# Kernel optimization log

Measured on AMD Instinct MI355X. Metric: run time of the kernel, lower is better.

Reference implementation:

```python
import jax, jax.numpy as jnp
import numpy as np

HIDDEN_DIM = 512
SCALE = float(np.sqrt(HIDDEN_DIM))  # hidden_dim ** 0.5, matches torch


def setup_inputs() -> dict:
    key = jax.random.key(0)
    ks = jax.random.split(key, 4)
    B, S, D_IN = 8, 4096, 64
    x = jax.random.normal(ks[0], (B, S, D_IN), dtype=jnp.float32)
    # Linear weights stored as [in, out] (transposed vs torch's [out, in])
    Wq = jax.random.normal(ks[1], (D_IN, HIDDEN_DIM), dtype=jnp.float32) * (1.0 / np.sqrt(D_IN))
    Wk = jax.random.normal(ks[2], (D_IN, HIDDEN_DIM), dtype=jnp.float32) * (1.0 / np.sqrt(D_IN))
    Wv = jax.random.normal(ks[3], (D_IN, HIDDEN_DIM), dtype=jnp.float32) * (1.0 / np.sqrt(D_IN))
    bq = jnp.zeros((HIDDEN_DIM,), dtype=jnp.float32)
    bk = jnp.zeros((HIDDEN_DIM,), dtype=jnp.float32)
    bv = jnp.zeros((HIDDEN_DIM,), dtype=jnp.float32)
    return {"x": x, "Wq": Wq, "bq": bq, "Wk": Wk, "bk": bk, "Wv": Wv, "bv": bv}


def reference(x, Wq, bq, Wk, bk, Wv, bv):
    # Q/K/V projections: [B, S, H]
    Q = jnp.einsum('bsd,dh->bsh', x, Wq) + bq
    K = jnp.einsum('bsd,dh->bsh', x, Wk) + bk
    V = jnp.einsum('bsd,dh->bsh', x, Wv) + bv
    # Naive single-head attention with full [B, S, S] score matrix,
    # matching the original torch math exactly.
    scores = jnp.einsum('bqh,bkh->bqk', Q, K) / SCALE
    attn = jax.nn.softmax(scores, axis=-1)
    return jnp.einsum('bqk,bkh->bqh', attn, V)
```

## Files before the change

### kernel.cpp

```cpp
#include <hip/hip_runtime.h>
#include <hip/hip_bf16.h>
#include <math.h>


#define SS 4096
#define DD 64
#define HH 512
#define KSPL 2048

#define CSCALE ((float)(1.4426950408889634 * 0.04419417382415922))

typedef __bf16 bf16x8 __attribute__((ext_vector_type(8)));
typedef float  f32x4  __attribute__((ext_vector_type(4)));
typedef unsigned int u32x4 __attribute__((ext_vector_type(4)));

__device__ __forceinline__ float b2f(__hip_bfloat16 v) { return __bfloat162float(v); }

__device__ __forceinline__ f32x4 mfma16(bf16x8 a, bf16x8 b, f32x4 c) {
  return __builtin_amdgcn_mfma_f32_16x16x32_bf16(a, b, c, 0, 0, 0);
}

__device__ __forceinline__ unsigned pack2(float a, float b) {
  float2 f2; f2.x = a; f2.y = b;
  __hip_bfloat162 h2 = __float22bfloat162_rn(f2);
  unsigned u; __builtin_memcpy(&u, &h2, 4);
  return u;
}

__device__ __forceinline__ float loadf(const void* p, size_t i, int isF32) {
  return isF32 ? ((const float*)p)[i] : b2f(((const __hip_bfloat16*)p)[i]);
}
__device__ __forceinline__ void load8f(const void* p, size_t i, int isF32, float* o) {
  if (isF32) {
    const float4 a = *(const float4*)((const float*)p + i);
    const float4 b = *(const float4*)((const float*)p + i + 4);
    o[0]=a.x; o[1]=a.y; o[2]=a.z; o[3]=a.w; o[4]=b.x; o[5]=b.y; o[6]=b.z; o[7]=b.w;
  } else {
    const bf16x8 v = *(const bf16x8*)((const __hip_bfloat16*)p + i);
#pragma unroll
    for (int k = 0; k < 8; ++k) { __hip_bfloat16 h; __builtin_memcpy(&h, ((const unsigned short*)&v) + k, 2); o[k] = b2f(h); }
  }
}

__global__ void dtype_probe(const void* __restrict__ Wq, int* __restrict__ flag) {
  const unsigned short* h = (const unsigned short*)Wq;
  const int lane = threadIdx.x;
  unsigned int bits = ((unsigned int)h[lane * 2]) << 16;
  float v; __builtin_memcpy(&v, &bits, 4);
  v = fabsf(v);
  if (!isfinite(v) || v > 1e10f) v = 1e10f;
  for (int off = 1; off < 64; off <<= 1) v = fmaxf(v, __shfl_xor(v, off, 64));
  if (lane == 0) *flag = (v > 1e6f) ? 1 : 0;
}

__global__ __launch_bounds__(256) void prep_kernel(
    const void* __restrict__ Wq, const void* __restrict__ Wk,
    const void* __restrict__ Wv, const void* __restrict__ bq,
    const void* __restrict__ bk, __hip_bfloat16* __restrict__ MT,
    float* __restrict__ u, float* __restrict__ w_, float* __restrict__ c_,
    __hip_bfloat16* __restrict__ wvT, const int* __restrict__ flag) {
  const int t = threadIdx.x, blk = blockIdx.x;
  const int isF32 = *flag;
  if (blk < 64) {
    __shared__ float red[256];
    const int i = blk, j = t >> 2, part = t & 3;
    float acc = 0.f, aq[8], ak[8];
    for (int c = 0; c < 16; ++c) {
      load8f(Wq, (size_t)i * HH + part * 128 + c * 8, isF32, aq);
      load8f(Wk, (size_t)j * HH + part * 128 + c * 8, isF32, ak);
#pragma unroll
      for (int k = 0; k < 8; ++k) acc = fmaf(aq[k], ak[k], acc);
    }
    red[t] = acc;
    __syncthreads();
    if (t < 64)
      MT[t * 64 + i] = __float2bfloat16(red[t*4] + red[t*4+1] + red[t*4+2] + red[t*4+3]);
  } else if (blk == 64) {
    __shared__ float pu[256], pw[256], pc[64];
    const int i = t & 63, part = t >> 6;
    float au = 0.f, aw = 0.f, v1[8], v2[8];
    for (int c = 0; c < 16; ++c) {
      load8f(Wq, (size_t)i * HH + part * 128 + c * 8, isF32, v1);
      load8f(bk, part * 128 + c * 8, isF32, v2);
#pragma unroll
      for (int k = 0; k < 8; ++k) au = fmaf(v1[k], v2[k], au);
      load8f(Wk, (size_t)i * HH + part * 128 + c * 8, isF32, v1);
      load8f(bq, part * 128 + c * 8, isF32, v2);
#pragma unroll
      for (int k = 0; k < 8; ++k) aw = fmaf(v1[k], v2[k], aw);
    }
    pu[t] = au; pw[t] = aw;
    if (t < 64) {
      float s = 0.f;
      for (int e = 0; e < 8; ++e)
        s = fmaf(loadf(bq, t * 8 + e, isF32), loadf(bk, t * 8 + e, isF32), s);
      pc[t] = s;
    }
    __syncthreads();
    if (t < 64) {
      u[t]  = pu[t] + pu[t+64] + pu[t+128] + pu[t+192];
      w_[t] = pw[t] + pw[t+64] + pw[t+128] + pw[t+192];
    }
    if (t == 0) {
      float s = 0.f;
      for (int e = 0; e < 64; ++e) s += pc[e];
      *c_ = s;
    }
  } else {
    const int base = (blk - 65) * 2048 + t;
    for (int r = 0; r < 8; ++r) {
      const int e = base + r * 256;
      const int h = e >> 6, d = e & 63;
      wvT[e] = __float2bfloat16(loadf(Wv, (size_t)d * HH + h, isF32));
    }
  }
}

__global__ __launch_bounds__(256) void proj_kernel(
    const void* __restrict__ xraw, const __hip_bfloat16* __restrict__ MT,
    const float* __restrict__ u, const float* __restrict__ w_,
    const float* __restrict__ c_, __hip_bfloat16* __restrict__ xc,
    __hip_bfloat16* __restrict__ y, float* __restrict__ qb,
    float* __restrict__ kb, __hip_bfloat16* __restrict__ xT,
    const int* __restrict__ flag) {
  __shared__ __hip_bfloat16 xs[64 * 72];
  __shared__ __hip_bfloat16 Ms[64 * 72];
  __shared__ float us[64], wl[64];
  __shared__ float cs;

  const int t = threadIdx.x;
  const int isF32 = *flag;
  {
    const int r = t >> 2, cb = (t & 3) * 16;
    *(bf16x8*)(&Ms[r * 72 + cb])     = *(const bf16x8*)(MT + r * 64 + cb);
    *(bf16x8*)(&Ms[r * 72 + cb + 8]) = *(const bf16x8*)(MT + r * 64 + cb + 8);
  }
  if (t < 64) { us[t] = u[t]; wl[t] = w_[t]; }
  if (t == 0) cs = *c_;

  const int b = blockIdx.x & 7;
  const int sbase = (blockIdx.x >> 3) * 64;
  const int rbase = b * SS + sbase;

  for (int i = 0; i < 2; ++i) {
    const int e = i * 256 + t;
    const int row = e >> 3, col = (e & 7) * 8;
    float v[8];
    load8f(xraw, (size_t)(rbase + row) * DD + col, isF32, v);
    __hip_bfloat16* dp = xs + row * 72 + col;
#pragma unroll
    for (int k = 0; k < 8; ++k) dp[k] = __float2bfloat16(v[k]);
  }
  __syncthreads();

  const int wv = t >> 6, lane = t & 63;
  const int l16 = lane & 15, quad = lane >> 4;
  const bf16x8 A0 = *(const bf16x8*)(&xs[(wv * 16 + l16) * 72 + quad * 8]);
  const bf16x8 A1 = *(const bf16x8*)(&xs[(wv * 16 + l16) * 72 + 32 + quad * 8]);
#pragma unroll
  for (int nt = 0; nt < 4; ++nt) {
    const bf16x8 B0 = *(const bf16x8*)(&Ms[(nt * 16 + l16) * 72 + quad * 8]);
    const bf16x8 B1 = *(const bf16x8*)(&Ms[(nt * 16 + l16) * 72 + 32 + quad * 8]);
    f32x4 C = (f32x4){0.f, 0.f, 0.f, 0.f};
    C = mfma16(A0, B0, C);
    C = mfma16(A1, B1, C);
#pragma unroll
    for (int r = 0; r < 4; ++r)
      y[(size_t)(rbase + wv * 16 + quad * 4 + r) * DD + nt * 16 + l16] =
          __float2bfloat16(C[r]);
  }
  if (t < 64) {
    float qa = 0.f, ka = 0.f;
    for (int d = 0; d < 64; ++d) {
      const float xv = b2f(xs[t * 72 + d]);
      qa = fmaf(xv, us[d], qa);
      ka = fmaf(xv, wl[d], ka);
    }
    qb[rbase + t] = (qa + cs) * CSCALE;
    kb[rbase + t] = ka * CSCALE;
  }
  for (int i = 0; i < 2; ++i) {
    const int e = i * 256 + t;
    const int row = e >> 3, col = (e & 7) * 8;
    *(bf16x8*)(xc + (size_t)(rbase + row) * DD + col) = *(const bf16x8*)(xs + row * 72 + col);
  }
  for (int i = 0; i < 16; ++i) {
    const int d = i * 4 + (t >> 6);
    const int sl = t & 63;
    xT[((size_t)b * DD + d) * SS + sbase + sl] = xs[sl * 72 + d];
  }
}

__global__ __launch_bounds__(256) void attn_split(
    const __hip_bfloat16* __restrict__ x,
    const __hip_bfloat16* __restrict__ y,
    const float* __restrict__ qb, const float* __restrict__ kb,
    const __hip_bfloat16* __restrict__ xT,
    float* __restrict__ Opart, float* __restrict__ lpart) {
  __shared__ __hip_bfloat16 xs[2][32 * 72];
  __shared__ __hip_bfloat16 vsm[2][64 * 40];
  const int tid = threadIdx.x;
  const int wv = tid >> 6, lane = tid & 63;
  const int l16 = lane & 15, quad = lane >> 4;
  const int b = blockIdx.x & 7;
  const int ks = (blockIdx.x >> 3) & 1;
  const int qt = (blockIdx.x >> 4) * 4 + wv;
  const int koff = ks * KSPL;
  const size_t rowq = ((size_t)b << 12) + ((size_t)qt << 4);

  const __hip_bfloat16* xb  = x  + ((size_t)b * SS) * DD;
  const __hip_bfloat16* xTb = xT + ((size_t)b * DD) * SS;
  const float* kbb = kb + ((size_t)b * SS);

  const __hip_bfloat16* yp = y + (rowq + l16) * DD + quad * 8;
  const bf16x8 Ylo = *(const bf16x8*)yp;
  const bf16x8 Yhi = *(const bf16x8*)(yp + 32);
  const float qbl = qb[rowq + l16];

  const int sxr = tid >> 3, sxc = (tid & 7) * 8;
  const int taur = (sxr & 3) + ((sxr >> 3) << 2) + (((sxr >> 2) & 1) << 4);
  const int svd = tid >> 2, svc = (tid & 3) * 8;
  const __hip_bfloat16* gx = xb + (size_t)(koff + sxr) * DD + sxc;
  const __hip_bfloat16* gv = xTb + (size_t)svd * SS + koff + svc;
  const float* kbp = kbb + koff + quad * 8;

  bf16x8 nx = *(const bf16x8*)gx;
  bf16x8 nv = *(const bf16x8*)gv;
  *(bf16x8*)(&xs[0][taur * 72 + sxc]) = nx;
  *(bf16x8*)(&vsm[0][svd * 40 + svc]) = nv;
  nx = *(const bf16x8*)(gx + 32 * DD);
  nv = *(const bf16x8*)(gv + 32);
  __syncthreads();

  bf16x8 onesb;
#pragma unroll
  for (int j = 0; j < 8; ++j) onesb[j] = (__bf16)1.0f;

  f32x4 O[4];
#pragma unroll
  for (int n = 0; n < 4; ++n) O[n] = (f32x4){0.f, 0.f, 0.f, 0.f};
  f32x4 Ol = (f32x4){0.f, 0.f, 0.f, 0.f};

  for (int kt = 0; kt < KSPL; kt += 32) {
    const int p = (kt >> 5) & 1, np = p ^ 1;
    if (kt + 32 < KSPL) {
      *(bf16x8*)(&xs[np][taur * 72 + sxc]) = nx;
      *(bf16x8*)(&vsm[np][svd * 40 + svc]) = nv;
      if (kt + 64 < KSPL) {
        nx = *(const bf16x8*)(gx + (size_t)(kt + 64) * DD);
        nv = *(const bf16x8*)(gv + (kt + 64));
      }
    }
    const f32x4 kb0 = *(const f32x4*)(kbp + kt);
    const f32x4 kb1 = *(const f32x4*)(kbp + kt + 4);

    const bf16x8 B00 = *(const bf16x8*)(&xs[p][l16 * 72 + quad * 8]);
    const bf16x8 B01 = *(const bf16x8*)(&xs[p][l16 * 72 + 32 + quad * 8]);
    const bf16x8 B10 = *(const bf16x8*)(&xs[p][(16 + l16) * 72 + quad * 8]);
    const bf16x8 B11 = *(const bf16x8*)(&xs[p][(16 + l16) * 72 + 32 + quad * 8]);
    const bf16x8 V0 = *(const bf16x8*)(&vsm[p][l16 * 40 + quad * 8]);
    const bf16x8 V1 = *(const bf16x8*)(&vsm[p][(16 + l16) * 40 + quad * 8]);
    const bf16x8 V2 = *(const bf16x8*)(&vsm[p][(32 + l16) * 40 + quad * 8]);
    const bf16x8 V3 = *(const bf16x8*)(&vsm[p][(48 + l16) * 40 + quad * 8]);

    f32x4 S0 = (f32x4){0.f, 0.f, 0.f, 0.f};
    f32x4 S1 = (f32x4){0.f, 0.f, 0.f, 0.f};
    S0 = mfma16(B00, Ylo, S0);
    S0 = mfma16(B01, Yhi, S0);
    S1 = mfma16(B10, Ylo, S1);
    S1 = mfma16(B11, Yhi, S1);

    float p0[4], p1[4];
#pragma unroll
    for (int r = 0; r < 4; ++r) {
      p0[r] = __builtin_amdgcn_exp2f(fmaf(S0[r], CSCALE, qbl + kb0[r]));
      p1[r] = __builtin_amdgcn_exp2f(fmaf(S1[r], CSCALE, qbl + kb1[r]));
    }
    u32x4 R;
    R[0] = pack2(p0[0], p0[1]);
    R[1] = pack2(p0[2], p0[3]);
    R[2] = pack2(p1[0], p1[1]);
    R[3] = pack2(p1[2], p1[3]);
    bf16x8 Pf;
    __builtin_memcpy(&Pf, &R, 16);

    O[0] = mfma16(Pf, V0, O[0]);
    O[1] = mfma16(Pf, V1, O[1]);
    O[2] = mfma16(Pf, V2, O[2]);
    O[3] = mfma16(Pf, V3, O[3]);
    Ol = mfma16(Pf, onesb, Ol);

    __syncthreads();
  }

  float* Op = Opart + ((size_t)ks * (SS * 8) + rowq) * 64;
#pragma unroll
  for (int n = 0; n < 4; ++n)
#pragma unroll
    for (int r = 0; r < 4; ++r)
      Op[(size_t)(quad * 4 + r) * 64 + n * 16 + l16] = O[n][r];
  if (l16 == 0) {
#pragma unroll
    for (int r = 0; r < 4; ++r)
      lpart[(size_t)ks * (SS * 8) + rowq + quad * 4 + r] = Ol[r];
  }
}

__global__ __launch_bounds__(256) void combine_kernel(
    const float* __restrict__ Opart, const float* __restrict__ lpart,
    const __hip_bfloat16* __restrict__ wvT, const void* __restrict__ bv_raw,
    void* __restrict__ out_raw, const int* __restrict__ flag) {
  const int tid = threadIdx.x;
  const int wv = tid >> 6, lane = tid & 63;
  const int l16 = lane & 15, quad = lane >> 4;
  const size_t q0 = (size_t)blockIdx.x * 64 + (size_t)wv * 16;
  const int isF32 = *flag;
  const size_t NP = (size_t)SS * 8;

  const float lsum = lpart[q0 + l16] + lpart[NP + q0 + l16];
  const float linv = (lsum > 0.f) ? 1.0f / lsum : 0.f;

  const float* p0 = Opart + (q0 + l16) * 64 + quad * 8;
  const float* p1 = p0 + NP * 64;
  float vlo[8], vhi[8];
#pragma unroll
  for (int j = 0; j < 8; j += 4) {
    const float4 a = *(const float4*)(p0 + j);
    const float4 b = *(const float4*)(p1 + j);
    vlo[j]   = (a.x + b.x) * linv; vlo[j+1] = (a.y + b.y) * linv;
    vlo[j+2] = (a.z + b.z) * linv; vlo[j+3] = (a.w + b.w) * linv;
    const float4 c = *(const float4*)(p0 + 32 + j);
    const float4 d = *(const float4*)(p1 + 32 + j);
    vhi[j]   = (c.x + d.x) * linv; vhi[j+1] = (c.y + d.y) * linv;
    vhi[j+2] = (c.z + d.z) * linv; vhi[j+3] = (c.w + d.w) * linv;
  }
  u32x4 Rlo, Rhi;
#pragma unroll
  for (int j = 0; j < 4; ++j) {
    Rlo[j] = pack2(vlo[2*j], vlo[2*j+1]);
    Rhi[j] = pack2(vhi[2*j], vhi[2*j+1]);
  }
  bf16x8 Alo, Ahi;
  __builtin_memcpy(&Alo, &Rlo, 16);
  __builtin_memcpy(&Ahi, &Rhi, 16);

  float* outf = (float*)out_raw;
  __hip_bfloat16* outb = (__hip_bfloat16*)out_raw;
#pragma unroll 4
  for (int ht = 0; ht < 32; ++ht) {
    const __hip_bfloat16* wp = wvT + (size_t)(ht * 16 + l16) * DD + quad * 8;
    const bf16x8 Wlo = *(const bf16x8*)wp;
    const bf16x8 Whi = *(const bf16x8*)(wp + 32);
    f32x4 C = (f32x4){0.f, 0.f, 0.f, 0.f};
    C = mfma16(Alo, Wlo, C);
    C = mfma16(Ahi, Whi, C);
    const float bvv = loadf(bv_raw, ht * 16 + l16, isF32);
#pragma unroll
    for (int r = 0; r < 4; ++r) {
      const size_t oidx = (q0 + quad * 4 + r) * HH + ht * 16 + l16;
      const float val = C[r] + bvv;
      if (isF32) outf[oidx] = val;
      else       outb[oidx] = __float2bfloat16(val);
    }
  }
}

__global__ __launch_bounds__(256) void attn_kernel(
    const __hip_bfloat16* __restrict__ x,
    const __hip_bfloat16* __restrict__ y,
    const float* __restrict__ qb, const float* __restrict__ kb,
    const __hip_bfloat16* __restrict__ xT,
    const __hip_bfloat16* __restrict__ wvT,
    const void* __restrict__ bv_raw,
    void* __restrict__ out_raw, const int* __restrict__ flag) {
  __shared__ __hip_bfloat16 xs[2][32 * 72];
  __shared__ __hip_bfloat16 vsm[2][64 * 40];
  __shared__ float kbl[SS];
  const int tid = threadIdx.x;
  const int wv = tid >> 6, lane = tid & 63;
  const int l16 = lane & 15, quad = lane >> 4;
  const int b = blockIdx.x & 7;
  const int qt = (blockIdx.x >> 3) * 4 + wv;
  const size_t rowq = ((size_t)b << 12) + ((size_t)qt << 4);
  const int isF32 = *flag;

  const __hip_bfloat16* xb  = x  + ((size_t)b * SS) * DD;
  const __hip_bfloat16* xTb = xT + ((size_t)b * DD) * SS;
  const float* kbb = kb + ((size_t)b * SS);

  const __hip_bfloat16* yp = y + (rowq + l16) * DD + quad * 8;
  const bf16x8 Ylo = *(const bf16x8*)yp;
  const bf16x8 Yhi = *(const bf16x8*)(yp + 32);
  const float qbl = qb[rowq + l16];

  const int sxr = tid >> 3, sxc = (tid & 7) * 8;
  const int taur = (sxr & 3) + ((sxr >> 3) << 2) + (((sxr >> 2) & 1) << 4);
  const int svd = tid >> 2, svc = (tid & 3) * 8;
  const __hip_bfloat16* gx = xb + (size_t)sxr * DD + sxc;
  const __hip_bfloat16* gv = xTb + (size_t)svd * SS + svc;

#pragma unroll
  for (int j = 0; j < 4; ++j) {
    const int c = j * 256 + tid;
    *(f32x4*)(&kbl[c * 4]) = *(const f32x4*)(kbb + c * 4);
  }

  bf16x8 nx = *(const bf16x8*)gx;
  bf16x8 nv = *(const bf16x8*)gv;
  *(bf16x8*)(&xs[0][taur * 72 + sxc]) = nx;
  *(bf16x8*)(&vsm[0][svd * 40 + svc]) = nv;
  nx = *(const bf16x8*)(gx + 32 * DD);
  nv = *(const bf16x8*)(gv + 32);
  __syncthreads();

  bf16x8 onesb;
#pragma unroll
  for (int j = 0; j < 8; ++j) onesb[j] = (__bf16)1.0f;

  f32x4 O[4];
#pragma unroll
  for (int n = 0; n < 4; ++n) O[n] = (f32x4){0.f, 0.f, 0.f, 0.f};
  f32x4 Ol = (f32x4){0.f, 0.f, 0.f, 0.f};

  for (int kt = 0; kt < SS; kt += 32) {
    const int p = (kt >> 5) & 1, np = p ^ 1;
    if (kt + 32 < SS) {
      *(bf16x8*)(&xs[np][taur * 72 + sxc]) = nx;
      *(bf16x8*)(&vsm[np][svd * 40 + svc]) = nv;
      if (kt + 64 < SS) {
        nx = *(const bf16x8*)(gx + (size_t)(kt + 64) * DD);
        nv = *(const bf16x8*)(gv + (kt + 64));
      }
    }
    const bf16x8 B00 = *(const bf16x8*)(&xs[p][l16 * 72 + quad * 8]);
    const bf16x8 B01 = *(const bf16x8*)(&xs[p][l16 * 72 + 32 + quad * 8]);
    const bf16x8 B10 = *(const bf16x8*)(&xs[p][(16 + l16) * 72 + quad * 8]);
    const bf16x8 B11 = *(const bf16x8*)(&xs[p][(16 + l16) * 72 + 32 + quad * 8]);
    const bf16x8 V0 = *(const bf16x8*)(&vsm[p][l16 * 40 + quad * 8]);
    const bf16x8 V1 = *(const bf16x8*)(&vsm[p][(16 + l16) * 40 + quad * 8]);
    const bf16x8 V2 = *(const bf16x8*)(&vsm[p][(32 + l16) * 40 + quad * 8]);
    const bf16x8 V3 = *(const bf16x8*)(&vsm[p][(48 + l16) * 40 + quad * 8]);

    f32x4 S0 = (f32x4){0.f, 0.f, 0.f, 0.f};
    f32x4 S1 = (f32x4){0.f, 0.f, 0.f, 0.f};
    S0 = mfma16(B00, Ylo, S0);
    S0 = mfma16(B01, Yhi, S0);
    S1 = mfma16(B10, Ylo, S1);
    S1 = mfma16(B11, Yhi, S1);

    const f32x4 kb0 = *(const f32x4*)(&kbl[kt + quad * 8]);
    const f32x4 kb1 = *(const f32x4*)(&kbl[kt + quad * 8 + 4]);

    float p0[4], p1[4];
#pragma unroll
    for (int r = 0; r < 4; ++r) {
      p0[r] = __builtin_amdgcn_exp2f(fmaf(S0[r], CSCALE, qbl + kb0[r]));
      p1[r] = __builtin_amdgcn_exp2f(fmaf(S1[r], CSCALE, qbl + kb1[r]));
    }
    u32x4 R;
    R[0] = pack2(p0[0], p0[1]);
    R[1] = pack2(p0[2], p0[3]);
    R[2] = pack2(p1[0], p1[1]);
    R[3] = pack2(p1[2], p1[3]);
    bf16x8 Pf;
    __builtin_memcpy(&Pf, &R, 16);

    O[0] = mfma16(Pf, V0, O[0]);
    O[1] = mfma16(Pf, V1, O[1]);
    O[2] = mfma16(Pf, V2, O[2]);
    O[3] = mfma16(Pf, V3, O[3]);
    Ol = mfma16(Pf, onesb, Ol);

    __syncthreads();
  }

  float inv_l[4];
#pragma unroll
  for (int r = 0; r < 4; ++r)
    inv_l[r] = (Ol[r] > 0.f) ? 1.0f / Ol[r] : 0.f;
  __hip_bfloat16* pl = &xs[0][0] + wv * 1152;
#pragma unroll
  for (int n = 0; n < 4; ++n)
#pragma unroll
    for (int r = 0; r < 4; ++r) {
      const int row = quad * 4 + r;
      pl[row * 72 + n * 16 + l16] = __float2bfloat16(O[n][r] * inv_l[r]);
    }
  __syncthreads();
  const bf16x8 Alo = *(const bf16x8*)(pl + l16 * 72 + quad * 8);
  const bf16x8 Ahi = *(const bf16x8*)(pl + l16 * 72 + 32 + quad * 8);

  float* outf = (float*)out_raw;
  __hip_bfloat16* outb = (__hip_bfloat16*)out_raw;
#pragma unroll 4
  for (int ht = 0; ht < 32; ++ht) {
    const __hip_bfloat16* wp = wvT + (size_t)(ht * 16 + l16) * DD + quad * 8;
    const bf16x8 Wlo = *(const bf16x8*)wp;
    const bf16x8 Whi = *(const bf16x8*)(wp + 32);
    f32x4 C = (f32x4){0.f, 0.f, 0.f, 0.f};
    C = mfma16(Alo, Wlo, C);
    C = mfma16(Ahi, Whi, C);
    const float bvv = loadf(bv_raw, ht * 16 + l16, isF32);
#pragma unroll
    for (int r = 0; r < 4; ++r) {
      const size_t oidx = (rowq + quad * 4 + r) * HH + ht * 16 + l16;
      const float val = C[r] + bvv;
      if (isF32) outf[oidx] = val;
      else       outb[oidx] = __float2bfloat16(val);
    }
  }
}

extern "C" void kernel_launch(void* const* d_in, const int* in_sizes, int n_in,
                              void* d_out, int out_size, void* d_ws,
                              size_t ws_size, hipStream_t stream) {
  char* ws = (char*)d_ws;
  int*   flag = (int*)(ws + 0);
  __hip_bfloat16* MT = (__hip_bfloat16*)(ws + 1024);
  float* u    = (float*)(ws + 9216);
  float* w_   = (float*)(ws + 9728);
  float* c_   = (float*)(ws + 10240);
  __hip_bfloat16* wvT = (__hip_bfloat16*)(ws + 32768);
  __hip_bfloat16* xc  = (__hip_bfloat16*)(ws + 131072);
  __hip_bfloat16* y   = (__hip_bfloat16*)(ws + 4325376);
  float* qb = (float*)(ws + 8519680);
  float* kb = (float*)(ws + 8650752);
  __hip_bfloat16* xT = (__hip_bfloat16*)(ws + 8781824);
  float* Opart = (float*)(ws + 16777216);
  float* lpart = (float*)(ws + 33554432);
  const size_t ws_need = 33816576;

  dtype_probe<<<1, 64, 0, stream>>>(d_in[1], flag);
  prep_kernel<<<81, 256, 0, stream>>>(d_in[1], d_in[3], d_in[5], d_in[2],
                                      d_in[4], MT, u, w_, c_, wvT, flag);
  proj_kernel<<<512, 256, 0, stream>>>(d_in[0], MT, u, w_, c_, xc, y, qb, kb,
                                       xT, flag);
  if (ws_size >= ws_need) {
    attn_split<<<1024, 256, 0, stream>>>(xc, y, qb, kb, xT, Opart, lpart);
    combine_kernel<<<512, 256, 0, stream>>>(Opart, lpart, wvT, d_in[6], d_out,
                                            flag);
  } else {
    attn_kernel<<<512, 256, 0, stream>>>(xc, y, qb, kb, xT, wvT, d_in[6],
                                         d_out, flag);
  }
}
```

Measured before the change: 190.1 us.

## Switch attention to 32x32 MFMA tiles with 4-way key split

Rewrites the split attention kernel to use 32x32x16 bf16 MFMA, giving each wave 32 query rows instead of 16. Each block now loads a K/V tile once for 128 queries instead of 64, and the row sums are accumulated in registers rather than through an extra MFMA against a ones vector. The key dimension is split four ways when the workspace allows it, and the combine kernel now sums over a variable number of partials. This roughly doubles the Opart traffic and raises register pressure from the 16-wide accumulators.

New measurement: 193.0 us. Within noise of the previous version (+1.6%).

```diff
diff --git a/kernel.cpp b/kernel.cpp
--- a/kernel.cpp
+++ b/kernel.cpp
@@ -6,18 +6,21 @@
 #define SS 4096
 #define DD 64
 #define HH 512
-#define KSPL 2048
 
 #define CSCALE ((float)(1.4426950408889634 * 0.04419417382415922))
 
 typedef __bf16 bf16x8 __attribute__((ext_vector_type(8)));
 typedef float  f32x4  __attribute__((ext_vector_type(4)));
+typedef float  f32x16 __attribute__((ext_vector_type(16)));
 typedef unsigned int u32x4 __attribute__((ext_vector_type(4)));
 
 __device__ __forceinline__ float b2f(__hip_bfloat16 v) { return __bfloat162float(v); }
 
 __device__ __forceinline__ f32x4 mfma16(bf16x8 a, bf16x8 b, f32x4 c) {
   return __builtin_amdgcn_mfma_f32_16x16x32_bf16(a, b, c, 0, 0, 0);
+}
+__device__ __forceinline__ f32x16 mfma32(bf16x8 a, bf16x8 b, f32x16 c) {
+  return __builtin_amdgcn_mfma_f32_32x32x16_bf16(a, b, c, 0, 0, 0);
 }
 
 __device__ __forceinline__ unsigned pack2(float a, float b) {
@@ -196,33 +199,33 @@
     const __hip_bfloat16* __restrict__ y,
     const float* __restrict__ qb, const float* __restrict__ kb,
     const __hip_bfloat16* __restrict__ xT,
-    float* __restrict__ Opart, float* __restrict__ lpart) {
+    float* __restrict__ Opart, float* __restrict__ lpart, int lgs) {
   __shared__ __hip_bfloat16 xs[2][32 * 72];
   __shared__ __hip_bfloat16 vsm[2][64 * 40];
   const int tid = threadIdx.x;
   const int wv = tid >> 6, lane = tid & 63;
-  const int l16 = lane & 15, quad = lane >> 4;
+  const int l32 = lane & 31, hi = lane >> 5;
   const int b = blockIdx.x & 7;
-  const int ks = (blockIdx.x >> 3) & 1;
-  const int qt = (blockIdx.x >> 4) * 4 + wv;
-  const int koff = ks * KSPL;
-  const size_t rowq = ((size_t)b << 12) + ((size_t)qt << 4);
-
-  const __hip_bfloat16* xb  = x  + ((size_t)b * SS) * DD;
-  const __hip_bfloat16* xTb = xT + ((size_t)b * DD) * SS;
-  const float* kbb = kb + ((size_t)b * SS);
-
-  const __hip_bfloat16* yp = y + (rowq + l16) * DD + quad * 8;
-  const bf16x8 Ylo = *(const bf16x8*)yp;
-  const bf16x8 Yhi = *(const bf16x8*)(yp + 32);
-  const float qbl = qb[rowq + l16];
+  const int nspl = 1 << lgs;
+  const int ks = (blockIdx.x >> 3) & (nspl - 1);
+  const int qg = blockIdx.x >> (3 + lgs);
+  const int kspl = SS >> lgs;
+  const int koff = ks * kspl;
+  const size_t rowq = ((size_t)b << 12) + (size_t)qg * 128 + wv * 32;
+
+  bf16x8 Y[4];
+#pragma unroll
+  for (int mi = 0; mi < 4; ++mi)
+    Y[mi] = *(const bf16x8*)(y + (rowq + l32) * DD + mi * 16 + hi * 8);
+  const float qbl = qb[rowq + l32];
 
   const int sxr = tid >> 3, sxc = (tid & 7) * 8;
-  const int taur = (sxr & 3) + ((sxr >> 3) << 2) + (((sxr >> 2) & 1) << 4);
+  const int g = sxr >> 2;
+  const int taur = (sxr & 3) + 4 * ((g & 4) | ((g & 1) << 1) | ((g >> 1) & 1));
   const int svd = tid >> 2, svc = (tid & 3) * 8;
-  const __hip_bfloat16* gx = xb + (size_t)(koff + sxr) * DD + sxc;
-  const __hip_bfloat16* gv = xTb + (size_t)svd * SS + koff + svc;
-  const float* kbp = kbb + koff + quad * 8;
+  const __hip_bfloat16* gx = x + ((size_t)b * SS + koff + sxr) * DD + sxc;
+  const __hip_bfloat16* gv = xT + ((size_t)b * DD + svd) * SS + koff + svc;
+  const float* kbp = kb + (size_t)b * SS + koff + hi * 8;
 
   bf16x8 nx = *(const bf16x8*)gx;
   bf16x8 nv = *(const bf16x8*)gv;
@@ -232,113 +235,122 @@
   nv = *(const bf16x8*)(gv + 32);
   __syncthreads();
 
-  bf16x8 onesb;
-#pragma unroll
-  for (int j = 0; j < 8; ++j) onesb[j] = (__bf16)1.0f;
-
-  f32x4 O[4];
-#pragma unroll
-  for (int n = 0; n < 4; ++n) O[n] = (f32x4){0.f, 0.f, 0.f, 0.f};
-  f32x4 Ol = (f32x4){0.f, 0.f, 0.f, 0.f};
-
-  for (int kt = 0; kt < KSPL; kt += 32) {
+  f32x16 O0, O1;
+#pragma unroll
+  for (int r = 0; r < 16; ++r) { O0[r] = 0.f; O1[r] = 0.f; }
+  float lp = 0.f;
+
+  for (int kt = 0; kt < kspl; kt += 32) {
     const int p = (kt >> 5) & 1, np = p ^ 1;
-    if (kt + 32 < KSPL) {
+    if (kt + 32 < kspl) {
       *(bf16x8*)(&xs[np][taur * 72 + sxc]) = nx;
       *(bf16x8*)(&vsm[np][svd * 40 + svc]) = nv;
-      if (kt + 64 < KSPL) {
+      if (kt + 64 < kspl) {
         nx = *(const bf16x8*)(gx + (size_t)(kt + 64) * DD);
         nv = *(const bf16x8*)(gv + (kt + 64));
       }
     }
-    const f32x4 kb0 = *(const f32x4*)(kbp + kt);
-    const f32x4 kb1 = *(const f32x4*)(kbp + kt + 4);
-
-    const bf16x8 B00 = *(const bf16x8*)(&xs[p][l16 * 72 + quad * 8]);
-    const bf16x8 B01 = *(const bf16x8*)(&xs[p][l16 * 72 + 32 + quad * 8]);
-    const bf16x8 B10 = *(const bf16x8*)(&xs[p][(16 + l16) * 72 + quad * 8]);
-    const bf16x8 B11 = *(const bf16x8*)(&xs[p][(16 + l16) * 72 + 32 + quad * 8]);
-    const bf16x8 V0 = *(const bf16x8*)(&vsm[p][l16 * 40 + quad * 8]);
-    const bf16x8 V1 = *(const bf16x8*)(&vsm[p][(16 + l16) * 40 + quad * 8]);
-    const bf16x8 V2 = *(const bf16x8*)(&vsm[p][(32 + l16) * 40 + quad * 8]);
-    const bf16x8 V3 = *(const bf16x8*)(&vsm[p][(48 + l16) * 40 + quad * 8]);
-
-    f32x4 S0 = (f32x4){0.f, 0.f, 0.f, 0.f};
-    f32x4 S1 = (f32x4){0.f, 0.f, 0.f, 0.f};
-    S0 = mfma16(B00, Ylo, S0);
-    S0 = mfma16(B01, Yhi, S0);
-    S1 = mfma16(B10, Ylo, S1);
-    S1 = mfma16(B11, Yhi, S1);
-
-    float p0[4], p1[4];
-#pragma unroll
-    for (int r = 0; r < 4; ++r) {
-      p0[r] = __builtin_amdgcn_exp2f(fmaf(S0[r], CSCALE, qbl + kb0[r]));
-      p1[r] = __builtin_amdgcn_exp2f(fmaf(S1[r], CSCALE, qbl + kb1[r]));
-    }
-    u32x4 R;
-    R[0] = pack2(p0[0], p0[1]);
-    R[1] = pack2(p0[2], p0[3]);
-    R[2] = pack2(p1[0], p1[1]);
-    R[3] = pack2(p1[2], p1[3]);
-    bf16x8 Pf;
-    __builtin_memcpy(&Pf, &R, 16);
-
-    O[0] = mfma16(Pf, V0, O[0]);
-    O[1] = mfma16(Pf, V1, O[1]);
-    O[2] = mfma16(Pf, V2, O[2]);
-    O[3] = mfma16(Pf, V3, O[3]);
-    Ol = mfma16(Pf, onesb, Ol);
+    const f32x4 kb0a = *(const f32x4*)(kbp + kt);
+    const f32x4 kb0b = *(const f32x4*)(kbp + kt + 4);
+    const f32x4 kb1a = *(const f32x4*)(kbp + kt + 16);
+    const f32x4 kb1b = *(const f32x4*)(kbp + kt + 20);
+
+    const bf16x8 A0 = *(const bf16x8*)(&xs[p][l32 * 72 + hi * 8]);
+    const bf16x8 A1 = *(const bf16x8*)(&xs[p][l32 * 72 + 16 + hi * 8]);
+    const bf16x8 A2 = *(const bf16x8*)(&xs[p][l32 * 72 + 32 + hi * 8]);
+    const bf16x8 A3 = *(const bf16x8*)(&xs[p][l32 * 72 + 48 + hi * 8]);
+
+    f32x16 S;
+#pragma unroll
+    for (int r = 0; r < 16; ++r) S[r] = 0.f;
+    S = mfma32(A0, Y[0], S);
+    S = mfma32(A1, Y[1], S);
+    S = mfma32(A2, Y[2], S);
+    S = mfma32(A3, Y[3], S);
+
+    float pv[16];
+#pragma unroll
+    for (int r = 0; r < 16; ++r) {
+      const float kv = (r < 4) ? kb0a[r & 3]
+                     : (r < 8) ? kb0b[r & 3]
+                     : (r < 12) ? kb1a[r & 3] : kb1b[r & 3];
+      pv[r] = __builtin_amdgcn_exp2f(fmaf(S[r], CSCALE, qbl + kv));
+    }
+    {
+      float s0 = (pv[0]+pv[1]) + (pv[2]+pv[3]);
+      float s1 = (pv[4]+pv[5]) + (pv[6]+pv[7]);
+      float s2 = (pv[8]+pv[9]) + (pv[10]+pv[11]);
+      float s3 = (pv[12]+pv[13]) + (pv[14]+pv[15]);
+      lp += (s0 + s1) + (s2 + s3);
+    }
+    u32x4 R0, R1;
+    R0[0] = pack2(pv[0], pv[1]);  R0[1] = pack2(pv[2], pv[3]);
+    R0[2] = pack2(pv[4], pv[5]);  R0[3] = pack2(pv[6], pv[7]);
+    R1[0] = pack2(pv[8], pv[9]);  R1[1] = pack2(pv[10], pv[11]);
+    R1[2] = pack2(pv[12], pv[13]); R1[3] = pack2(pv[14], pv[15]);
+    bf16x8 Pf0, Pf1;
+    __builtin_memcpy(&Pf0, &R0, 16);
+    __builtin_memcpy(&Pf1, &R1, 16);
+
+    const bf16x8 V00 = *(const bf16x8*)(&vsm[p][l32 * 40 + hi * 8]);
+    const bf16x8 V10 = *(const bf16x8*)(&vsm[p][l32 * 40 + 16 + hi * 8]);
+    const bf16x8 V01 = *(const bf16x8*)(&vsm[p][(l32 + 32) * 40 + hi * 8]);
+    const bf16x8 V11 = *(const bf16x8*)(&vsm[p][(l32 + 32) * 40 + 16 + hi * 8]);
+
+    O0 = mfma32(Pf0, V00, O0);
+    O0 = mfma32(Pf1, V10, O0);
+    O1 = mfma32(Pf0, V01, O1);
+    O1 = mfma32(Pf1, V11, O1);
 
     __syncthreads();
   }
 
-  float* Op = Opart + ((size_t)ks * (SS * 8) + rowq) * 64;
-#pragma unroll
-  for (int n = 0; n < 4; ++n)
-#pragma unroll
-    for (int r = 0; r < 4; ++r)
-      Op[(size_t)(quad * 4 + r) * 64 + n * 16 + l16] = O[n][r];
-  if (l16 == 0) {
-#pragma unroll
-    for (int r = 0; r < 4; ++r)
-      lpart[(size_t)ks * (SS * 8) + rowq + quad * 4 + r] = Ol[r];
-  }
-}
-
-__global__ __launch_bounds__(256) void combine_kernel(
+  lp += __shfl_xor(lp, 32, 64);
+  const size_t NP = (size_t)SS * 8;
+  if (hi == 0) lpart[(size_t)ks * NP + rowq + l32] = lp;
+
+  float* Op = Opart + ((size_t)ks * NP + rowq) * 64;
+#pragma unroll
+  for (int r = 0; r < 16; ++r) {
+    const int qrow = (r & 3) + 8 * (r >> 2) + 4 * hi;
+    Op[(size_t)qrow * 64 + l32]      = O0[r];
+    Op[(size_t)qrow * 64 + 32 + l32] = O1[r];
+  }
+}
+
+__global__ __launch_bounds__(128) void combine_kernel(
     const float* __restrict__ Opart, const float* __restrict__ lpart,
     const __hip_bfloat16* __restrict__ wvT, const void* __restrict__ bv_raw,
-    void* __restrict__ out_raw, const int* __restrict__ flag) {
+    void* __restrict__ out_raw, const int* __restrict__ flag, int nspl) {
   const int tid = threadIdx.x;
   const int wv = tid >> 6, lane = tid & 63;
   const int l16 = lane & 15, quad = lane >> 4;
-  const size_t q0 = (size_t)blockIdx.x * 64 + (size_t)wv * 16;
+  const size_t q0 = (size_t)blockIdx.x * 32 + (size_t)wv * 16;
   const int isF32 = *flag;
   const size_t NP = (size_t)SS * 8;
 
-  const float lsum = lpart[q0 + l16] + lpart[NP + q0 + l16];
+  float lsum = 0.f;
+  for (int s = 0; s < nspl; ++s) lsum += lpart[(size_t)s * NP + q0 + l16];
   const float linv = (lsum > 0.f) ? 1.0f / lsum : 0.f;
 
-  const float* p0 = Opart + (q0 + l16) * 64 + quad * 8;
-  const float* p1 = p0 + NP * 64;
   float vlo[8], vhi[8];
 #pragma unroll
-  for (int j = 0; j < 8; j += 4) {
-    const float4 a = *(const float4*)(p0 + j);
-    const float4 b = *(const float4*)(p1 + j);
-    vlo[j]   = (a.x + b.x) * linv; vlo[j+1] = (a.y + b.y) * linv;
-    vlo[j+2] = (a.z + b.z) * linv; vlo[j+3] = (a.w + b.w) * linv;
-    const float4 c = *(const float4*)(p0 + 32 + j);
-    const float4 d = *(const float4*)(p1 + 32 + j);
-    vhi[j]   = (c.x + d.x) * linv; vhi[j+1] = (c.y + d.y) * linv;
-    vhi[j+2] = (c.z + d.z) * linv; vhi[j+3] = (c.w + d.w) * linv;
+  for (int j = 0; j < 8; ++j) { vlo[j] = 0.f; vhi[j] = 0.f; }
+  for (int s = 0; s < nspl; ++s) {
+    const float* p0 = Opart + ((size_t)s * NP + q0 + l16) * 64 + quad * 8;
+#pragma unroll
+    for (int j = 0; j < 8; j += 4) {
+      const float4 a = *(const float4*)(p0 + j);
+      vlo[j]   += a.x; vlo[j+1] += a.y; vlo[j+2] += a.z; vlo[j+3] += a.w;
+      const float4 c = *(const float4*)(p0 + 32 + j);
+      vhi[j]   += c.x; vhi[j+1] += c.y; vhi[j+2] += c.z; vhi[j+3] += c.w;
+    }
   }
   u32x4 Rlo, Rhi;
 #pragma unroll
   for (int j = 0; j < 4; ++j) {
-    Rlo[j] = pack2(vlo[2*j], vlo[2*j+1]);
-    Rhi[j] = pack2(vhi[2*j], vhi[2*j+1]);
+    Rlo[j] = pack2(vlo[2*j] * linv, vlo[2*j+1] * linv);
+    Rhi[j] = pack2(vhi[2*j] * linv, vhi[2*j+1] * linv);
   }
   bf16x8 Alo, Ahi;
   __builtin_memcpy(&Alo, &Rlo, 16);
@@ -527,18 +539,25 @@
   float* kb = (float*)(ws + 8650752);
   __hip_bfloat16* xT = (__hip_bfloat16*)(ws + 8781824);
   float* Opart = (float*)(ws + 16777216);
-  float* lpart = (float*)(ws + 33554432);
-  const size_t ws_need = 33816576;
+  const size_t NP = (size_t)SS * 8;
+  const size_t need4 = 16777216UL + 4UL * NP * 64 * 4 + 4UL * NP * 4;
+  const size_t need2 = 16777216UL + 2UL * NP * 64 * 4 + 2UL * NP * 4;
 
   dtype_probe<<<1, 64, 0, stream>>>(d_in[1], flag);
   prep_kernel<<<81, 256, 0, stream>>>(d_in[1], d_in[3], d_in[5], d_in[2],
                                       d_in[4], MT, u, w_, c_, wvT, flag);
   proj_kernel<<<512, 256, 0, stream>>>(d_in[0], MT, u, w_, c_, xc, y, qb, kb,
                                        xT, flag);
-  if (ws_size >= ws_need) {
-    attn_split<<<1024, 256, 0, stream>>>(xc, y, qb, kb, xT, Opart, lpart);
-    combine_kernel<<<512, 256, 0, stream>>>(Opart, lpart, wvT, d_in[6], d_out,
-                                            flag);
+  if (ws_size >= need4) {
+    float* lpart = (float*)(ws + 16777216 + 4UL * NP * 64 * 4);
+    attn_split<<<1024, 256, 0, stream>>>(xc, y, qb, kb, xT, Opart, lpart, 2);
+    combine_kernel<<<1024, 128, 0, stream>>>(Opart, lpart, wvT, d_in[6], d_out,
+                                             flag, 4);
+  } else if (ws_size >= need2) {
+    float* lpart = (float*)(ws + 16777216 + 2UL * NP * 64 * 4);
+    attn_split<<<512, 256, 0, stream>>>(xc, y, qb, kb, xT, Opart, lpart, 1);
+    combine_kernel<<<1024, 128, 0, stream>>>(Opart, lpart, wvT, d_in[6], d_out,
+                                             flag, 2);
   } else {
     attn_kernel<<<512, 256, 0, stream>>>(xc, y, qb, kb, xT, wvT, d_in[6],
                                          d_out, flag);
```
